# Optimization experiments

Hardware: AMD Instinct MI355X
Metric: run time of the kernel (lower is better)

The kernel has to match this reference:

```python
import jax, jax.numpy as jnp
import numpy as np

N = 50000; E = 120000; FN = 64; EA = 16; R = 4; H = 4; HID = 128; L = 3
NIDS = 10001; IDE = 32; RED = 8; NG = 64; NC = 10; KH = 128; GRID = 5; ORD = 3
EDIM = EA + RED; FFH = 256; GK = GRID + ORD


def layernorm(x, w, b):
    m = x.mean(-1, keepdims=True)
    v = ((x - m) ** 2).mean(-1, keepdims=True)
    return (x - m) / jnp.sqrt(v + 1e-5) * w + b


def b_splines(x, grid, k):
    # x: (B, in); grid: (in, G + 2k + 1) -> bases: (B, in, G + k)
    xe = x[..., None]
    bases = ((xe >= grid[:, :-1]) & (xe < grid[:, 1:])).astype(x.dtype)
    for j in range(1, k + 1):
        bases = ((xe - grid[:, :-(j + 1)]) / (grid[:, j:-1] - grid[:, :-(j + 1)]) * bases[..., :-1]
                 + (grid[:, j + 1:] - xe) / (grid[:, j + 1:] - grid[:, 1:-j]) * bases[..., 1:])
    return bases


def kan_linear(x, bw, sw, sc, grid):
    base = jax.nn.silu(x) @ bw.T
    B = b_splines(x, grid, ORD)
    return base + jnp.einsum('big,oig->bo', B, sw * sc[..., None])


def make_grid(in_features):
    h = 2.0 / GRID
    g = np.arange(-ORD, GRID + ORD + 1) * h - 1.0
    return jnp.asarray(np.tile(g, (in_features, 1)), dtype=jnp.float32)


def setup_inputs():
    key = jax.random.key(0)
    ks = jax.random.split(key, 24)
    s = 0.02
    inp = {}
    inp['x'] = jax.random.normal(ks[0], (N, FN), jnp.float32)
    inp['edge_attr'] = jax.random.normal(ks[1], (E, EA), jnp.float32)
    inp['id_token'] = jax.random.randint(ks[2], (N,), 0, NIDS)
    inp['edge_index'] = jax.random.randint(ks[3], (2, E), 0, N)
    inp['edge_type'] = jax.random.randint(ks[4], (E,), 0, R)
    inp['batch'] = jnp.sort(jax.random.randint(ks[5], (N,), 0, NG))
    inp['id_emb_table'] = jax.random.normal(ks[6], (NIDS, IDE)) * s
    inp['in_proj_w'] = jax.random.normal(ks[7], (HID, FN + IDE)) * s
    inp['in_proj_b'] = jnp.zeros((HID,))
    inp['rel_emb'] = jax.random.normal(ks[8], (L, R, RED)) * s
    inp['lin_l_w'] = jax.random.normal(ks[9], (L, R, H * HID, HID)) * s
    inp['lin_l_b'] = jnp.zeros((L, R, H * HID))
    inp['lin_r_w'] = jax.random.normal(ks[10], (L, R, H * HID, HID)) * s
    inp['lin_r_b'] = jnp.zeros((L, R, H * HID))
    inp['lin_edge_w'] = jax.random.normal(ks[11], (L, R, H * HID, EDIM)) * s
    inp['att_w'] = jax.random.normal(ks[12], (L, R, H, HID)) * s
    inp['conv_bias'] = jnp.zeros((L, R, HID))
    inp['rel_gate'] = jnp.zeros((L, R))
    inp['norm1_w'] = jnp.ones((L, HID)); inp['norm1_b'] = jnp.zeros((L, HID))
    inp['norm2_w'] = jnp.ones((L, HID)); inp['norm2_b'] = jnp.zeros((L, HID))
    inp['ffn_w1'] = jax.random.normal(ks[13], (L, FFH, HID)) * s
    inp['ffn_b1'] = jnp.zeros((L, FFH))
    inp['ffn_w2'] = jax.random.normal(ks[14], (L, HID, FFH)) * s
    inp['ffn_b2'] = jnp.zeros((L, HID))
    inp['readout_norm_w'] = jnp.ones((2 * HID,)); inp['readout_norm_b'] = jnp.zeros((2 * HID,))
    inp['base_w1'] = jax.random.normal(ks[15], (KH, 2 * HID)) * s
    inp['spline_w1'] = jax.random.normal(ks[16], (KH, 2 * HID, GK)) * s
    inp['spline_scaler1'] = jnp.ones((KH, 2 * HID))
    inp['grid1'] = make_grid(2 * HID)
    inp['base_w2'] = jax.random.normal(ks[17], (NC, KH)) * s
    inp['spline_w2'] = jax.random.normal(ks[18], (NC, KH, GK)) * s
    inp['spline_scaler2'] = jnp.ones((NC, KH))
    inp['grid2'] = make_grid(KH)
    return inp


def reference(x, edge_attr, id_token, edge_index, edge_type, batch,
              id_emb_table, in_proj_w, in_proj_b, rel_emb,
              lin_l_w, lin_l_b, lin_r_w, lin_r_b, lin_edge_w, att_w, conv_bias,
              rel_gate, norm1_w, norm1_b, norm2_w, norm2_b,
              ffn_w1, ffn_b1, ffn_w2, ffn_b2, readout_norm_w, readout_norm_b,
              base_w1, spline_w1, spline_scaler1, grid1,
              base_w2, spline_w2, spline_scaler2, grid2):
    src, dst = edge_index[0], edge_index[1]
    h = jnp.concatenate([x, id_emb_table[id_token]], -1)
    h = jax.nn.silu(h @ in_proj_w.T + in_proj_b)  # input_proj (eval: no dropout)
    for l in range(L):
        gate = jax.nn.softmax(rel_gate[l])  # all relations present w.h.p.
        h_msg = jnp.zeros_like(h)
        for r in range(R):
            maskf = (edge_type == r).astype(h.dtype)
            ea = jnp.concatenate([edge_attr, jnp.broadcast_to(rel_emb[l, r], (E, RED))], -1)
            xl = (h @ lin_l_w[l, r].T + lin_l_b[l, r]).reshape(N, H, HID)
            xr = (h @ lin_r_w[l, r].T + lin_r_b[l, r]).reshape(N, H, HID)
            ee = (ea @ lin_edge_w[l, r].T).reshape(E, H, HID)
            sfeat = jax.nn.leaky_relu(xl[src] + xr[dst] + ee, negative_slope=0.2)
            logit = jnp.einsum('ehc,hc->eh', sfeat, att_w[l, r])
            logit = jnp.where(maskf[:, None] > 0, logit, -1e9)
            m = jax.ops.segment_max(logit, dst, num_segments=N)
            a = jnp.exp(logit - m[dst]) * maskf[:, None]
            den = jax.ops.segment_sum(a, dst, num_segments=N)
            a = a / jnp.where(den == 0, 1.0, den)[dst]
            out = jax.ops.segment_sum(a[:, :, None] * xl[src], dst, num_segments=N)
            out = out.mean(1) + conv_bias[l, r]  # concat=False -> head mean
            h_msg = h_msg + gate[r] * out
        h = layernorm(h + h_msg, norm1_w[l], norm1_b[l])
        f = jax.nn.silu(h @ ffn_w1[l].T + ffn_b1[l]) @ ffn_w2[l].T + ffn_b2[l]
        h = layernorm(h + f, norm2_w[l], norm2_b[l])
    cnt = jax.ops.segment_sum(jnp.ones((N,), h.dtype), batch, num_segments=NG)
    hmean = jax.ops.segment_sum(h, batch, num_segments=NG) / jnp.maximum(cnt, 1.0)[:, None]
    hmax = jax.ops.segment_max(h, batch, num_segments=NG)
    g = layernorm(jnp.concatenate([hmean, hmax], -1), readout_norm_w, readout_norm_b)
    z = kan_linear(g, base_w1, spline_w1, spline_scaler1, grid1)
    logits = kan_linear(z, base_w2, spline_w2, spline_scaler2, grid2)
    return logits
```

## Files before the change

### kernel.cpp

```cpp
#include <hip/hip_runtime.h>
#include <math.h>

#define NN 50000
#define NE 120000
#define FN 64
#define NEA 16
#define NR 4
#define NH 4
#define HID 128
#define NL 3
#define IDE 32
#define RED 8
#define NG 64
#define NC 10
#define KH 128
#define FFH 256
#define NBIN (NR * NN)
#define SCAN_BLK ((NBIN + 1023) / 1024)
#define CAPS 32768
#define CAPH 9216

typedef short bf16x8 __attribute__((ext_vector_type(8)));
typedef float f32x4 __attribute__((ext_vector_type(4)));

__device__ __forceinline__ unsigned short f2b(float f) {
  unsigned u = __float_as_uint(f);
  unsigned r = (u + 0x7FFFu + ((u >> 16) & 1u)) >> 16;
  return (unsigned short)r;
}
__device__ __forceinline__ float b2f(unsigned short b) {
  return __uint_as_float((unsigned)b << 16);
}

__global__ void cvt_bf16(const float* __restrict__ s, unsigned short* __restrict__ d, int n4) {
  int i = blockIdx.x * blockDim.x + threadIdx.x;
  if (i >= n4) return;
  float4 v = ((const float4*)s)[i];
  ushort4 o;
  o.x = f2b(v.x); o.y = f2b(v.y); o.z = f2b(v.z); o.w = f2b(v.w);
  ((ushort4*)d)[i] = o;
}

template <int KT>
__device__ __forceinline__ void gemm_direct(
    const unsigned short* __restrict__ A, const int* __restrict__ rowlist,
    const unsigned short* __restrict__ W, const float* __restrict__ bias,
    float* __restrict__ Cf, unsigned short* __restrict__ Cb,
    int nrows, int mout, int act, int rowBase, int colBase) {
  constexpr int NK = KT / 32;
  __shared__ unsigned short Es[64][136];
  int t = threadIdx.x;
  int lane = t & 63, w = t >> 6;
  int wm = w >> 1, wn = w & 1;
  int q = lane >> 4, mr = lane & 15;

  const unsigned short* ap[2];
#pragma unroll
  for (int mt = 0; mt < 2; ++mt) {
    int gr = rowBase + wm * 32 + mt * 16 + mr;
    int cg = (gr < nrows) ? gr : 0;
    int ar = rowlist ? rowlist[cg] : cg;
    ap[mt] = A + (size_t)ar * KT + q * 8;
  }
  const unsigned short* wp[4];
#pragma unroll
  for (int nt = 0; nt < 4; ++nt)
    wp[nt] = W + (size_t)(colBase + wn * 64 + nt * 16 + mr) * KT + q * 8;

  f32x4 acc[2][4] = {};
#pragma unroll
  for (int k = 0; k < NK; ++k) {
    bf16x8 af[2], bfr[4];
#pragma unroll
    for (int mt = 0; mt < 2; ++mt) af[mt] = *(const bf16x8*)(ap[mt] + k * 32);
#pragma unroll
    for (int nt = 0; nt < 4; ++nt) bfr[nt] = *(const bf16x8*)(wp[nt] + k * 32);
#pragma unroll
    for (int mt = 0; mt < 2; ++mt)
#pragma unroll
      for (int nt = 0; nt < 4; ++nt)
        acc[mt][nt] = __builtin_amdgcn_mfma_f32_16x16x32_bf16(af[mt], bfr[nt], acc[mt][nt], 0, 0, 0);
  }

  float bv[4];
#pragma unroll
  for (int nt = 0; nt < 4; ++nt) bv[nt] = bias[colBase + wn * 64 + nt * 16 + mr];

  if (Cf) {
#pragma unroll
    for (int mt = 0; mt < 2; ++mt)
#pragma unroll
      for (int nt = 0; nt < 4; ++nt)
#pragma unroll
        for (int r = 0; r < 4; ++r) {
          int row = rowBase + wm * 32 + mt * 16 + q * 4 + r;
          int col = colBase + wn * 64 + nt * 16 + mr;
          if (row < nrows) {
            float v = acc[mt][nt][r] + bv[nt];
            if (act) v = v / (1.f + expf(-v));
            Cf[(size_t)row * mout + col] = v;
            if (Cb) Cb[(size_t)row * mout + col] = f2b(v);
          }
        }
  } else {
#pragma unroll
    for (int mt = 0; mt < 2; ++mt)
#pragma unroll
      for (int nt = 0; nt < 4; ++nt)
#pragma unroll
        for (int r = 0; r < 4; ++r) {
          float v = acc[mt][nt][r] + bv[nt];
          if (act) v = v / (1.f + expf(-v));
          Es[wm * 32 + mt * 16 + q * 4 + r][wn * 64 + nt * 16 + mr] = f2b(v);
        }
    __syncthreads();
    int rl = t >> 2, co = (t & 3) * 32;
    int grow = rowBase + rl;
    if (grow < nrows) {
      unsigned short* dst = Cb + (size_t)grow * mout + colBase + co;
#pragma unroll
      for (int j = 0; j < 4; ++j)
        *(bf16x8*)(dst + j * 8) = *(const bf16x8*)&Es[rl][co + j * 8];
    }
  }
}

template <int KT>
__global__ __launch_bounds__(256, 2) void gemm_bf16_t(
    const unsigned short* __restrict__ A, const unsigned short* __restrict__ W,
    const float* __restrict__ bias, float* __restrict__ Cf, unsigned short* __restrict__ Cb,
    int nrows, int mout, int act, int ncol) {
  int nbr = (nrows + 63) >> 6;
  int rpx = (nbr + 7) >> 3;
  int xcd = blockIdx.x & 7, j = blockIdx.x >> 3;
  int rowT = xcd * rpx + j / ncol;
  int cy = j - (j / ncol) * ncol;
  if (rowT >= nbr) return;
  gemm_direct<KT>(A, nullptr, W, bias, Cf, Cb, nrows, mout, act, rowT * 64, cy * 128);
}

__global__ __launch_bounds__(256, 2) void conv_solo_all(
    const unsigned short* __restrict__ hbf,
    const int* __restrict__ srclist, const int* __restrict__ hotlist,
    const int* __restrict__ cnts,
    const unsigned short* __restrict__ Wl, const float* __restrict__ bl,
    const unsigned short* __restrict__ Wr, const float* __restrict__ br,
    unsigned short* __restrict__ xlb, unsigned short* __restrict__ xrh,
    const int* __restrict__ solosrc, const int* __restrict__ solodst,
    const unsigned short* __restrict__ wsum, const float* __restrict__ bsum,
    const float* __restrict__ gate, float* __restrict__ hmsg) {
  int t = threadIdx.x, lane = t & 63, w = t >> 6;
  int wm = w >> 1, wn = w & 1, q = lane >> 4, mr = lane & 15;
  for (int tid = blockIdx.x;; tid += gridDim.x) {
    int rem = tid, seg = 0, nrows = 0;
    for (; seg < 12; ++seg) {
      int n, tseg;
      if (seg < 8) {
        int r = seg >> 1;
        n = (seg & 1) ? cnts[64 + r * 16] : cnts[128 + r * 16];
        int cap = (seg & 1) ? CAPH : CAPS;
        if (n > cap) n = cap;
        tseg = ((n + 63) >> 6) * 4;
      } else {
        n = cnts[(seg - 8) * 16];
        tseg = (n + 63) >> 6;
      }
      if (rem < tseg) { nrows = n; break; }
      rem -= tseg;
    }
    if (seg == 12) return;
    if (seg < 8) {
      int r = seg >> 1, sel = seg & 1;
      int rt = rem >> 2, ct = rem & 3;
      const int* list = (sel ? hotlist : srclist) + r * NN;
      const unsigned short* W = (sel ? Wr : Wl) + (size_t)r * 512 * 128;
      const float* bias = (sel ? br : bl) + (size_t)r * 512;
      unsigned short* C = sel ? (xrh + (size_t)r * CAPH * 512) : (xlb + (size_t)r * CAPS * 512);
      gemm_direct<128>(hbf, list, W, bias, nullptr, C, nrows, 512, 0, rt * 64, ct * 128);
    } else {
      int r = seg - 8;
      int rowBase = rem * 64;
      const unsigned short* ap[2];
#pragma unroll
      for (int mt = 0; mt < 2; ++mt) {
        int gr = rowBase + wm * 32 + mt * 16 + mr;
        int idx = (gr < nrows) ? solosrc[r * NN + gr] : 0;
        ap[mt] = hbf + (size_t)idx * HID + q * 8;
      }
      const unsigned short* wp[4];
#pragma unroll
      for (int nt = 0; nt < 4; ++nt)
        wp[nt] = wsum + (size_t)r * 16384 + (size_t)(wn * 64 + nt * 16 + mr) * HID + q * 8;
      f32x4 acc[2][4] = {};
#pragma unroll
      for (int k = 0; k < 4; ++k) {
        bf16x8 af[2], bfr[4];
#pragma unroll
        for (int mt = 0; mt < 2; ++mt) af[mt] = *(const bf16x8*)(ap[mt] + k * 32);
#pragma unroll
        for (int nt = 0; nt < 4; ++nt) bfr[nt] = *(const bf16x8*)(wp[nt] + k * 32);
#pragma unroll
        for (int mt = 0; mt < 2; ++mt)
#pragma unroll
          for (int nt = 0; nt < 4; ++nt)
            acc[mt][nt] = __builtin_amdgcn_mfma_f32_16x16x32_bf16(af[mt], bfr[nt], acc[mt][nt], 0, 0, 0);
      }
      float g4 = gate[r] * 0.25f;
      float bv[4];
#pragma unroll
      for (int nt = 0; nt < 4; ++nt) bv[nt] = bsum[r * 128 + wn * 64 + nt * 16 + mr];
#pragma unroll
      for (int mt = 0; mt < 2; ++mt)
#pragma unroll
        for (int rr = 0; rr < 4; ++rr) {
          int row = rowBase + wm * 32 + mt * 16 + q * 4 + rr;
          if (row < nrows) {
            int dst = solodst[r * NN + row];
#pragma unroll
            for (int nt = 0; nt < 4; ++nt) {
              int col = wn * 64 + nt * 16 + mr;
              atomicAdd(&hmsg[(size_t)dst * HID + col], g4 * (acc[mt][nt][rr] + bv[nt]));
            }
          }
        }
    }
    __syncthreads();
  }
}

__global__ void wsum_build(const float* __restrict__ linlw, const float* __restrict__ linlb,
                           unsigned short* __restrict__ wsum, float* __restrict__ bsum) {
  int i = blockIdx.x * blockDim.x + threadIdx.x;
  if (i >= NL * NR * 128 * 128) return;
  int k = i & 127, o = (i >> 7) & 127, lr = i >> 14;
  float s = 0.f;
#pragma unroll
  for (int h = 0; h < NH; ++h) s += linlw[((size_t)lr * 512 + h * 128 + o) * 128 + k];
  wsum[i] = f2b(s);
  if (k == 0) {
    float b = 0.f;
#pragma unroll
    for (int h = 0; h < NH; ++h) b += linlb[(size_t)lr * 512 + h * 128 + o];
    bsum[lr * 128 + o] = b;
  }
}

__global__ __launch_bounds__(256, 2) void layer_tail(
    float* __restrict__ h, float* __restrict__ hmsg, const float* __restrict__ cb,
    const float* __restrict__ n1w, const float* __restrict__ n1b,
    const unsigned short* __restrict__ W1, const float* __restrict__ b1,
    const unsigned short* __restrict__ W2, const float* __restrict__ b2,
    const float* __restrict__ n2w, const float* __restrict__ n2b,
    unsigned short* __restrict__ hbfout) {
  __shared__ __align__(16) char smem[64 * 136 * 2 + 64 * 264 * 2];
  unsigned short (*Y)[136] = (unsigned short (*)[136])smem;
  unsigned short (*F1)[264] = (unsigned short (*)[264])(smem + 64 * 136 * 2);
  float (*Ef)[132] = (float (*)[132])(smem + 64 * 136 * 2);
  int nbr = (NN + 63) >> 6;
  int rpx = (nbr + 7) >> 3;
  int xcd = blockIdx.x & 7, j = blockIdx.x >> 3;
  int rowT = xcd * rpx + j;
  if (rowT >= nbr) return;
  int rowBase = rowT * 64;

  int t = threadIdx.x;
  int lane = t & 63, w = t >> 6;
  int wm = w >> 1, wn = w & 1;
  int q = lane >> 4, mr = lane & 15;

  float y0r[16], y1r[16];
  {
    float w0 = n1w[lane], w1 = n1w[64 + lane];
    float bb0 = n1b[lane], bb1 = n1b[64 + lane];
    float c0 = cb[lane], c1 = cb[64 + lane];
#pragma unroll
    for (int it = 0; it < 16; ++it) {
      int rr = it * 4 + w;
      int grow = rowBase + rr;
      if (grow < NN) {
        size_t base = (size_t)grow * HID;
        float x0 = h[base + lane] + hmsg[base + lane] + c0;
        float x1 = h[base + 64 + lane] + hmsg[base + 64 + lane] + c1;
        hmsg[base + lane] = 0.f;
        hmsg[base + 64 + lane] = 0.f;
        float s = x0 + x1;
#pragma unroll
        for (int o = 32; o > 0; o >>= 1) s += __shfl_xor(s, o, 64);
        float mean = s * (1.f / 128.f);
        float d0 = x0 - mean, d1 = x1 - mean;
        float v = d0 * d0 + d1 * d1;
#pragma unroll
        for (int o = 32; o > 0; o >>= 1) v += __shfl_xor(v, o, 64);
        float inv = 1.f / sqrtf(v * (1.f / 128.f) + 1e-5f);
        float y0 = d0 * inv * w0 + bb0;
        float y1 = d1 * inv * w1 + bb1;
        y0r[it] = y0;
        y1r[it] = y1;
        Y[rr][lane] = f2b(y0);
        Y[rr][64 + lane] = f2b(y1);
      } else {
        y0r[it] = 0.f;
        y1r[it] = 0.f;
        Y[rr][lane] = 0;
        Y[rr][64 + lane] = 0;
      }
    }
  }
  __syncthreads();

  bf16x8 a[2][4];
#pragma unroll
  for (int mt = 0; mt < 2; ++mt)
#pragma unroll
    for (int k = 0; k < 4; ++k)
      a[mt][k] = *(const bf16x8*)&Y[wm * 32 + mt * 16 + mr][k * 32 + q * 8];

#pragma unroll
  for (int ph = 0; ph < 2; ++ph) {
    const unsigned short* wp[4];
#pragma unroll
    for (int nt = 0; nt < 4; ++nt)
      wp[nt] = W1 + (size_t)(ph * 128 + wn * 64 + nt * 16 + mr) * HID + q * 8;
    f32x4 acc[2][4] = {};
#pragma unroll
    for (int k = 0; k < 4; ++k) {
      bf16x8 bfr[4];
#pragma unroll
      for (int nt = 0; nt < 4; ++nt) bfr[nt] = *(const bf16x8*)(wp[nt] + k * 32);
#pragma unroll
      for (int mt = 0; mt < 2; ++mt)
#pragma unroll
        for (int nt = 0; nt < 4; ++nt)
          acc[mt][nt] = __builtin_amdgcn_mfma_f32_16x16x32_bf16(a[mt][k], bfr[nt], acc[mt][nt], 0, 0, 0);
    }
    float bv[4];
#pragma unroll
    for (int nt = 0; nt < 4; ++nt) bv[nt] = b1[ph * 128 + wn * 64 + nt * 16 + mr];
#pragma unroll
    for (int mt = 0; mt < 2; ++mt)
#pragma unroll
      for (int nt = 0; nt < 4; ++nt)
#pragma unroll
        for (int r = 0; r < 4; ++r) {
          float v = acc[mt][nt][r] + bv[nt];
          v = v / (1.f + expf(-v));
          F1[wm * 32 + mt * 16 + q * 4 + r][ph * 128 + wn * 64 + nt * 16 + mr] = f2b(v);
        }
  }
  __syncthreads();

  const unsigned short* wp2[4];
#pragma unroll
  for (int nt = 0; nt < 4; ++nt)
    wp2[nt] = W2 + (size_t)(wn * 64 + nt * 16 + mr) * FFH + q * 8;
  f32x4 acc2[2][4] = {};
#pragma unroll
  for (int k = 0; k < 8; ++k) {
    bf16x8 af[2], bfr[4];
#pragma unroll
    for (int mt = 0; mt < 2; ++mt)
      af[mt] = *(const bf16x8*)&F1[wm * 32 + mt * 16 + mr][k * 32 + q * 8];
#pragma unroll
    for (int nt = 0; nt < 4; ++nt) bfr[nt] = *(const bf16x8*)(wp2[nt] + k * 32);
#pragma unroll
    for (int mt = 0; mt < 2; ++mt)
#pragma unroll
      for (int nt = 0; nt < 4; ++nt)
        acc2[mt][nt] = __builtin_amdgcn_mfma_f32_16x16x32_bf16(af[mt], bfr[nt], acc2[mt][nt], 0, 0, 0);
  }
  __syncthreads();

  float bv2[4];
#pragma unroll
  for (int nt = 0; nt < 4; ++nt) bv2[nt] = b2[wn * 64 + nt * 16 + mr];
#pragma unroll
  for (int mt = 0; mt < 2; ++mt)
#pragma unroll
    for (int nt = 0; nt < 4; ++nt)
#pragma unroll
      for (int r = 0; r < 4; ++r)
        Ef[wm * 32 + mt * 16 + q * 4 + r][wn * 64 + nt * 16 + mr] = acc2[mt][nt][r] + bv2[nt];
  __syncthreads();

  float w0 = n2w[lane], w1 = n2w[64 + lane];
  float bb0 = n2b[lane], bb1 = n2b[64 + lane];
#pragma unroll
  for (int it = 0; it < 16; ++it) {
    int rr = it * 4 + w;
    int grow = rowBase + rr;
    if (grow >= NN) continue;
    size_t base = (size_t)grow * HID;
    float x0 = y0r[it] + Ef[rr][lane];
    float x1 = y1r[it] + Ef[rr][64 + lane];
    float s = x0 + x1;
#pragma unroll
    for (int o = 32; o > 0; o >>= 1) s += __shfl_xor(s, o, 64);
    float mean = s * (1.f / 128.f);
    float d0 = x0 - mean, d1 = x1 - mean;
    float v = d0 * d0 + d1 * d1;
#pragma unroll
    for (int o = 32; o > 0; o >>= 1) v += __shfl_xor(v, o, 64);
    float inv = 1.f / sqrtf(v * (1.f / 128.f) + 1e-5f);
    float y0 = d0 * inv * w0 + bb0;
    float y1 = d1 * inv * w1 + bb1;
    h[base + lane] = y0;
    h[base + 64 + lane] = y1;
    hbfout[base + lane] = f2b(y0);
    hbfout[base + 64 + lane] = f2b(y1);
  }
}

__global__ void build_xin_bf(const float* __restrict__ x, const int* __restrict__ idtok,
                             const float* __restrict__ emb, unsigned short* __restrict__ xin) {
  int i = blockIdx.x * blockDim.x + threadIdx.x;
  if (i >= NN * 96) return;
  int n = i / 96, k = i - n * 96;
  float v = (k < FN) ? x[(size_t)n * FN + k] : emb[(size_t)idtok[n] * IDE + (k - FN)];
  xin[i] = f2b(v);
}

__global__ void hist_bin(const int* __restrict__ ei, const int* __restrict__ et,
                         int* __restrict__ bcnt) {
  int e = blockIdx.x * blockDim.x + threadIdx.x;
  if (e >= NE) return;
  atomicAdd(&bcnt[et[e] * NN + ei[NE + e]], 1);
}
__global__ __launch_bounds__(256) void scan1(const int* __restrict__ cnt,
                                             int* __restrict__ pos, int* __restrict__ bsum) {
  __shared__ int lds[256];
  int b = blockIdx.x, t = threadIdx.x;
  int base = b * 1024 + t * 4;
  int v[4];
#pragma unroll
  for (int j = 0; j < 4; ++j) v[j] = (base + j < NBIN) ? cnt[base + j] : 0;
  int tot = v[0] + v[1] + v[2] + v[3];
  lds[t] = tot;
  __syncthreads();
  for (int off = 1; off < 256; off <<= 1) {
    int x = (t >= off) ? lds[t - off] : 0;
    __syncthreads();
    lds[t] += x;
    __syncthreads();
  }
  if (t == 255) bsum[b] = lds[255];
  int run = lds[t] - tot;
#pragma unroll
  for (int j = 0; j < 4; ++j) {
    if (base + j < NBIN) pos[base + j] = run;
    run += v[j];
  }
}
__global__ __launch_bounds__(256) void scan2(int* __restrict__ bsum) {
  __shared__ int lds[256];
  int t = threadIdx.x;
  int v = (t < SCAN_BLK) ? bsum[t] : 0;
  lds[t] = v;
  __syncthreads();
  for (int off = 1; off < 256; off <<= 1) {
    int x = (t >= off) ? lds[t - off] : 0;
    __syncthreads();
    lds[t] += x;
    __syncthreads();
  }
  if (t < SCAN_BLK) bsum[t] = lds[t] - v;
}
__global__ void scan3(int* __restrict__ pos, const int* __restrict__ bsum,
                      const int* __restrict__ cnt) {
  int i = blockIdx.x * blockDim.x + threadIdx.x;
  if (i >= NBIN) return;
  pos[i] += bsum[i >> 10];
  if (i == NBIN - 1) pos[NBIN] = pos[i] + cnt[i];
}
__global__ void scatter_bin(const int* __restrict__ ei, const int* __restrict__ et,
                            const int* __restrict__ csroff, int* __restrict__ cur,
                            int* __restrict__ elist) {
  int e = blockIdx.x * blockDim.x + threadIdx.x;
  if (e >= NE) return;
  int bin = et[e] * NN + ei[NE + e];
  int p = atomicAdd(&cur[bin], 1);
  elist[csroff[bin] + p] = e;
}
__global__ void sort_bins(const int* __restrict__ csroff, int* __restrict__ elist) {
  int b = blockIdx.x * blockDim.x + threadIdx.x;
  if (b >= NBIN) return;
  int s = csroff[b], e = csroff[b + 1];
  for (int i = s + 1; i < e; ++i) {
    int key = elist[i];
    int j = i - 1;
    while (j >= s && elist[j] > key) { elist[j + 1] = elist[j]; --j; }
    elist[j + 1] = key;
  }
}
__global__ void gather_edge(const int* __restrict__ ei, const int* __restrict__ elist,
                            const float* __restrict__ eattr,
                            int* __restrict__ rsrc, float* __restrict__ eacsr) {
  int p = blockIdx.x * blockDim.x + threadIdx.x;
  if (p >= NE) return;
  int e = elist[p];
  rsrc[p] = ei[e];
  const float4* s = (const float4*)(eattr + (size_t)e * NEA);
  float4* d = (float4*)(eacsr + (size_t)p * NEA);
#pragma unroll
  for (int j = 0; j < 4; ++j) d[j] = s[j];
}
__global__ void mark_hotsrc(const int* __restrict__ csroff, const int* __restrict__ rsrc,
                            int* __restrict__ srcflag) {
  int b = blockIdx.x * blockDim.x + threadIdx.x;
  if (b >= NBIN) return;
  int s = csroff[b], e = csroff[b + 1];
  if (e - s < 2) return;
  int rel = b / NN;
  for (int p = s; p < e; ++p) srcflag[rel * NN + rsrc[p]] = 1;
}
__global__ void build_src_o(const int* __restrict__ srcflag, const int* __restrict__ srcpos,
                            int* __restrict__ srclist, int* __restrict__ srcmap) {
  int b = blockIdx.x * blockDim.x + threadIdx.x;
  if (b >= NBIN) return;
  if (srcflag[b]) {
    int rel = b / NN;
    int pos = srcpos[b] - srcpos[rel * NN];
    srcmap[b] = pos;
    srclist[rel * NN + pos] = b - rel * NN;
  }
}
__global__ void fincnt(const int* __restrict__ srcpos, int* __restrict__ nsrc) {
  int r = threadIdx.x;
  if (r < NR) nsrc[r * 16] = srcpos[(r + 1) * NN] - srcpos[r * NN];
}
__global__ void remap_rsrc(const int* __restrict__ csroff, const int* __restrict__ rsrc,
                           const int* __restrict__ srcmap, int* __restrict__ rsrcx) {
  int p = blockIdx.x * blockDim.x + threadIdx.x;
  if (p >= NE) return;
  int rel = (p >= csroff[NN]) + (p >= csroff[2 * NN]) + (p >= csroff[3 * NN]);
  rsrcx[p] = srcmap[rel * NN + rsrc[p]];
}
__global__ __launch_bounds__(256) void build_hot(
    const int* __restrict__ csroff, const int* __restrict__ rsrc,
    int* __restrict__ nsolo, int* __restrict__ nhot,
    int* __restrict__ solosrc, int* __restrict__ solodst, int* __restrict__ hotlist) {
  __shared__ int wsc[4][4], whc[4][4];
  __shared__ int sbase[4], hbase[4];
  int t = threadIdx.x, wave = t >> 6, lane = t & 63;
  int b = blockIdx.x * 256 + t;
  bool valid = b < NBIN;
  int cnt = 0, rel = 0, s = 0;
  if (valid) { s = csroff[b]; cnt = csroff[b + 1] - s; rel = b / NN; }
  bool solo = valid && cnt == 1;
  bool hot = valid && cnt >= 2;
#pragma unroll
  for (int rr = 0; rr < 4; ++rr) {
    unsigned long long ms = __ballot(solo && rel == rr);
    unsigned long long mh = __ballot(hot && rel == rr);
    if (lane == 0) { wsc[wave][rr] = __popcll(ms); whc[wave][rr] = __popcll(mh); }
  }
  __syncthreads();
  if (t < 4) {
    int ssum = wsc[0][t] + wsc[1][t] + wsc[2][t] + wsc[3][t];
    int hsum = whc[0][t] + whc[1][t] + whc[2][t] + whc[3][t];
    sbase[t] = ssum ? atomicAdd(&nsolo[t * 16], ssum) : 0;
    hbase[t] = hsum ? atomicAdd(&nhot[t * 16], hsum) : 0;
  }
  __syncthreads();
#pragma unroll
  for (int rr = 0; rr < 4; ++rr) {
    unsigned long long ms = __ballot(solo && rel == rr);
    if (solo && rel == rr) {
      int before = 0;
#pragma unroll
      for (int wv = 0; wv < 4; ++wv) if (wv < wave) before += wsc[wv][rr];
      int pos = sbase[rr] + before + __popcll(ms & ((1ull << lane) - 1ull));
      solosrc[rr * NN + pos] = rsrc[s];
      solodst[rr * NN + pos] = b - rr * NN;
    }
    unsigned long long mh = __ballot(hot && rel == rr);
    if (hot && rel == rr) {
      int before = 0;
#pragma unroll
      for (int wv = 0; wv < 4; ++wv) if (wv < wave) before += whc[wv][rr];
      int pos = hbase[rr] + before + __popcll(mh & ((1ull << lane) - 1ull));
      hotlist[rr * NN + pos] = b - rr * NN;
    }
  }
}

__global__ void gate_cb_all(const float* __restrict__ rg, const float* __restrict__ cbias,
                            float* __restrict__ gate, float* __restrict__ cb) {
  __shared__ float g[NR];
  int l = blockIdx.x, t = threadIdx.x;
  const float* rgl = rg + l * NR;
  if (t == 0) {
    float mx = rgl[0];
    for (int r = 1; r < NR; ++r) mx = fmaxf(mx, rgl[r]);
    float s = 0.f, tmp[NR];
    for (int r = 0; r < NR; ++r) { tmp[r] = expf(rgl[r] - mx); s += tmp[r]; }
    for (int r = 0; r < NR; ++r) { g[r] = tmp[r] / s; gate[l * NR + r] = g[r]; }
  }
  __syncthreads();
  float c = 0.f;
  for (int r = 0; r < NR; ++r) c += g[r] * cbias[(size_t)l * NR * HID + r * HID + t];
  cb[l * HID + t] = c;
}

__global__ __launch_bounds__(256) void edge_all(
    const int* __restrict__ csroff, const int* __restrict__ rsrcx,
    const float* __restrict__ eacsr, const float* __restrict__ relembp,
    const float* __restrict__ wedgep, const float* __restrict__ attwp,
    const unsigned short* __restrict__ xlb, const unsigned short* __restrict__ xrh,
    const int* __restrict__ hotlist, const int* __restrict__ nhot,
    float* __restrict__ hmsg, const float* __restrict__ gate, int rel) {
  __shared__ float lds[4][128];
  int wave = threadIdx.x >> 6, lane = threadIdx.x & 63;
  float g4 = gate[rel] * 0.25f;
  int hh = wave;
  float wreg[2][24], areg[2];
#pragma unroll
  for (int j = 0; j < 2; ++j) {
    int col = hh * 128 + j * 64 + lane;
    const float* wp = wedgep + (size_t)col * 24;
#pragma unroll
    for (int k = 0; k < 24; ++k) wreg[j][k] = wp[k];
    areg[j] = attwp[col];
  }
  float evr0 = 0.f, evr1 = 0.f;
#pragma unroll
  for (int k = 0; k < 8; ++k) {
    float rk = relembp[k];
    evr0 += rk * wreg[0][NEA + k];
    evr1 += rk * wreg[1][NEA + k];
  }
  int nh = nhot[rel * 16];
  for (int wi = blockIdx.x; wi < nh; wi += gridDim.x) {
    int dst = hotlist[rel * NN + wi];
    int s = csroff[rel * NN + dst], e = csroff[rel * NN + dst + 1];
    {
      const unsigned short* xrp = xrh + (size_t)wi * 512;
      float xr0 = b2f(xrp[hh * 128 + lane]);
      float xr1 = b2f(xrp[hh * 128 + 64 + lane]);
      float m = -3.4e38f, den = 0.f, acc0 = 0.f, acc1 = 0.f;
      for (int p = s; p < e; ++p) {
        int src = rsrcx[p];
        const float* eap = eacsr + (size_t)p * NEA;
        float eev0 = evr0, eev1 = evr1;
#pragma unroll
        for (int k = 0; k < NEA; ++k) {
          float er = eap[k];
          eev0 += er * wreg[0][k];
          eev1 += er * wreg[1][k];
        }
        float xl0 = b2f(xlb[(size_t)src * 512 + hh * 128 + lane]);
        float xl1 = b2f(xlb[(size_t)src * 512 + hh * 128 + 64 + lane]);
        float s0 = xl0 + xr0 + eev0; s0 = (s0 > 0.f) ? s0 : 0.2f * s0;
        float s1 = xl1 + xr1 + eev1; s1 = (s1 > 0.f) ? s1 : 0.2f * s1;
        float lg = s0 * areg[0] + s1 * areg[1];
#pragma unroll
        for (int o = 32; o > 0; o >>= 1) lg += __shfl_xor(lg, o, 64);
        float mn = fmaxf(m, lg);
        float sc = expf(m - mn);
        float ex = expf(lg - mn);
        den = den * sc + ex;
        acc0 = acc0 * sc + ex * xl0;
        acc1 = acc1 * sc + ex * xl1;
        m = mn;
      }
      float wgt = g4 / den;
      lds[wave][lane] = acc0 * wgt;
      lds[wave][64 + lane] = acc1 * wgt;
    }
    __syncthreads();
    if (wave < 2) {
      int d = wave * 64 + lane;
      float v = lds[0][d] + lds[1][d] + lds[2][d] + lds[3][d];
      hmsg[(size_t)dst * HID + d] += v;
    }
    __syncthreads();
  }
}

__global__ void group_bounds(const int* __restrict__ batch, int* __restrict__ gstart) {
  int g = threadIdx.x + blockIdx.x * blockDim.x;
  if (g > NG) return;
  int lo = 0, hi = NN;
  while (lo < hi) {
    int mid = (lo + hi) >> 1;
    if (batch[mid] < g) lo = mid + 1; else hi = mid;
  }
  gstart[g] = lo;
}
__global__ __launch_bounds__(128) void readout_part2(
    const float* __restrict__ h, const int* __restrict__ gstart,
    float* __restrict__ psum, float* __restrict__ pmax) {
  int g = blockIdx.x, s = blockIdx.y, t = threadIdx.x;
  int r0 = gstart[g], r1 = gstart[g + 1];
  float acc = 0.f, mx = -3.4e38f;
  for (int row = r0 + s; row < r1; row += 8) {
    float v = h[(size_t)row * HID + t];
    acc += v;
    mx = fmaxf(mx, v);
  }
  psum[((size_t)g * 8 + s) * HID + t] = acc;
  pmax[((size_t)g * 8 + s) * HID + t] = mx;
}
__global__ __launch_bounds__(256) void readout_final(
    const int* __restrict__ gstart, const float* __restrict__ psum,
    const float* __restrict__ pmax, const float* __restrict__ w,
    const float* __restrict__ b, float* __restrict__ g) {
  int bg = blockIdx.x, t = threadIdx.x;
  __shared__ float red[256];
  float c = fmaxf((float)(gstart[bg + 1] - gstart[bg]), 1.f);
  float x;
  if (t < HID) {
    float ssum = 0.f;
    for (int s = 0; s < 8; ++s) ssum += psum[((size_t)bg * 8 + s) * HID + t];
    x = ssum / c;
  } else {
    float mx = -3.4e38f;
    for (int s = 0; s < 8; ++s) mx = fmaxf(mx, pmax[((size_t)bg * 8 + s) * HID + (t - HID)]);
    x = mx;
  }
  red[t] = x;
  __syncthreads();
  for (int s = 128; s > 0; s >>= 1) {
    if (t < s) red[t] += red[t + s];
    __syncthreads();
  }
  float mean = red[0] * (1.f / 256.f);
  __syncthreads();
  float d = x - mean;
  red[t] = d * d;
  __syncthreads();
  for (int s = 128; s > 0; s >>= 1) {
    if (t < s) red[t] += red[t + s];
    __syncthreads();
  }
  float inv = 1.f / sqrtf(red[0] * (1.f / 256.f) + 1e-5f);
  g[(size_t)bg * 256 + t] = d * inv * w[t] + b[t];
}

__device__ __forceinline__ void bspline8(float x, const float* __restrict__ t,
                                         float* __restrict__ out) {
  float bs[11];
#pragma unroll
  for (int j = 0; j < 11; ++j) bs[j] = (x >= t[j] && x < t[j + 1]) ? 1.f : 0.f;
#pragma unroll
  for (int k = 1; k <= 3; ++k) {
    for (int j = 0; j < 11 - k; ++j) {
      bs[j] = (x - t[j]) / (t[j + k] - t[j]) * bs[j] +
              (t[j + k + 1] - x) / (t[j + k + 1] - t[j + 1]) * bs[j + 1];
    }
  }
#pragma unroll
  for (int j = 0; j < 8; ++j) out[j] = bs[j];
}

__global__ __launch_bounds__(128) void kan1_part(
    const float* __restrict__ g, const float* __restrict__ bw,
    const float* __restrict__ sw, const float* __restrict__ sc,
    const float* __restrict__ grid, float* __restrict__ zpart) {
  int bg = blockIdx.x, ch = blockIdx.y, t = threadIdx.x;
  int base = ch * 32;
  __shared__ float B[32][8];
  __shared__ float sg[32];
  if (t < 32) {
    float x = g[(size_t)bg * 256 + base + t];
    sg[t] = x / (1.f + expf(-x));
    bspline8(x, grid + (size_t)(base + t) * 12, B[t]);
  }
  __syncthreads();
  float acc = 0.f;
  for (int i = 0; i < 32; ++i) {
    int col = base + i;
    acc += sg[i] * bw[(size_t)t * 256 + col];
    const float* swp = sw + ((size_t)t * 256 + col) * 8;
    float sp = 0.f;
#pragma unroll
    for (int k = 0; k < 8; ++k) sp += B[i][k] * swp[k];
    acc += sp * sc[(size_t)t * 256 + col];
  }
  zpart[((size_t)ch * NG + bg) * KH + t] = acc;
}

__global__ __launch_bounds__(128) void kan2(
    const float* __restrict__ zpart, const float* __restrict__ bw,
    const float* __restrict__ sw, const float* __restrict__ sc,
    const float* __restrict__ grid, float* __restrict__ out) {
  int bg = blockIdx.x, t = threadIdx.x;
  __shared__ float B[128][8];
  __shared__ float sz[128];
  float x = 0.f;
  for (int ch = 0; ch < 8; ++ch) x += zpart[((size_t)ch * NG + bg) * KH + t];
  sz[t] = x / (1.f + expf(-x));
  bspline8(x, grid + (size_t)t * 12, B[t]);
  __syncthreads();
  if (t < NC) {
    float acc = 0.f;
    for (int i = 0; i < 128; ++i) {
      acc += sz[i] * bw[(size_t)t * 128 + i];
      const float* swp = sw + ((size_t)t * 128 + i) * 8;
      float sp = 0.f;
#pragma unroll
      for (int k = 0; k < 8; ++k) sp += B[i][k] * swp[k];
      acc += sp * sc[(size_t)t * 128 + i];
    }
    out[(size_t)bg * NC + t] = acc;
  }
}

extern "C" void kernel_launch(void* const* d_in, const int* in_sizes, int n_in,
                              void* d_out, int out_size, void* d_ws, size_t ws_size,
                              hipStream_t stream) {
  const float* x       = (const float*)d_in[0];
  const float* eattr   = (const float*)d_in[1];
  const int*   idtok   = (const int*)d_in[2];
  const int*   ei      = (const int*)d_in[3];
  const int*   etype   = (const int*)d_in[4];
  const int*   batch   = (const int*)d_in[5];
  const float* idemb   = (const float*)d_in[6];
  const float* inw     = (const float*)d_in[7];
  const float* inb     = (const float*)d_in[8];
  const float* relemb  = (const float*)d_in[9];
  const float* linlw   = (const float*)d_in[10];
  const float* linlb   = (const float*)d_in[11];
  const float* linrw   = (const float*)d_in[12];
  const float* linrb   = (const float*)d_in[13];
  const float* linew   = (const float*)d_in[14];
  const float* attw    = (const float*)d_in[15];
  const float* convb   = (const float*)d_in[16];
  const float* relgate = (const float*)d_in[17];
  const float* n1w     = (const float*)d_in[18];
  const float* n1b     = (const float*)d_in[19];
  const float* n2w     = (const float*)d_in[20];
  const float* n2b     = (const float*)d_in[21];
  const float* f1w     = (const float*)d_in[22];
  const float* f1bias  = (const float*)d_in[23];
  const float* f2w     = (const float*)d_in[24];
  const float* f2bias  = (const float*)d_in[25];
  const float* rnw     = (const float*)d_in[26];
  const float* rnb     = (const float*)d_in[27];
  const float* bw1     = (const float*)d_in[28];
  const float* sw1     = (const float*)d_in[29];
  const float* sc1     = (const float*)d_in[30];
  const float* grid1   = (const float*)d_in[31];
  const float* bw2     = (const float*)d_in[32];
  const float* sw2     = (const float*)d_in[33];
  const float* sc2     = (const float*)d_in[34];
  const float* grid2   = (const float*)d_in[35];
  float* out = (float*)d_out;
  (void)in_sizes; (void)n_in; (void)out_size; (void)ws_size;

  char* p = (char*)d_ws;
  auto alloc = [&](size_t bytes) { void* q = (void*)p; p += (bytes + 255) & ~(size_t)255; return q; };
  float* h    = (float*)alloc((size_t)NN * HID * 4);
  float* hmsg = (float*)alloc((size_t)NN * HID * 4);
  unsigned short* hbf = (unsigned short*)alloc((size_t)NN * HID * 2);
  unsigned short* xlb = (unsigned short*)alloc((size_t)NR * CAPS * 512 * 2);
  unsigned short* xrh = (unsigned short*)alloc((size_t)NR * CAPH * 512 * 2);
  int* elist = (int*)alloc((size_t)NE * 4);
  int* rsrc  = (int*)alloc((size_t)NE * 4);
  int* rsrcx = (int*)alloc((size_t)NE * 4);
  float* eacsr = (float*)alloc((size_t)NE * NEA * 4);
  int* bcnt  = (int*)alloc((size_t)NBIN * 8 + 8);
  int* cur   = bcnt + NBIN;
  int* csroff = (int*)alloc((size_t)(NBIN + 1) * 4);
  int* srcpos = (int*)alloc((size_t)(NBIN + 1) * 4);
  int* bsum  = (int*)alloc((size_t)SCAN_BLK * 4);
  int* hotlist = (int*)alloc((size_t)NR * NN * 4);
  int* solosrc = (int*)alloc((size_t)NR * NN * 4);
  int* solodst = (int*)alloc((size_t)NR * NN * 4);
  int* srclist = (int*)alloc((size_t)NR * NN * 4);
  int* srcflag = (int*)alloc((size_t)NBIN * 4);
  int* srcmap  = (int*)alloc((size_t)NBIN * 4);
  int* cnts    = (int*)alloc(1024);
  int* nsolo   = cnts;
  int* nhot    = cnts + 64;
  int* nsrc    = cnts + 128;
  unsigned short* linlwb = (unsigned short*)alloc((size_t)NL * NR * 512 * 128 * 2);
  unsigned short* linrwb = (unsigned short*)alloc((size_t)NL * NR * 512 * 128 * 2);
  unsigned short* f1wb   = (unsigned short*)alloc((size_t)NL * 256 * 128 * 2);
  unsigned short* f2wb   = (unsigned short*)alloc((size_t)NL * 128 * 256 * 2);
  unsigned short* inwb   = (unsigned short*)alloc((size_t)128 * 96 * 2);
  unsigned short* wsumb  = (unsigned short*)alloc((size_t)NL * NR * 128 * 128 * 2);
  float* bsumf = (float*)alloc((size_t)NL * NR * 128 * 4);
  float* gate = (float*)alloc(NL * NR * 4);
  float* cb   = (float*)alloc(NL * HID * 4);
  int* gstart = (int*)alloc((size_t)(NG + 1) * 4);
  float* psum = (float*)alloc((size_t)NG * 8 * HID * 4);
  float* pmax = (float*)alloc((size_t)NG * 8 * HID * 4);
  float* zpart = (float*)alloc((size_t)8 * NG * KH * 4);
  float* g = (float*)alloc((size_t)NG * 256 * 4);
  unsigned short* xinbf = xlb;

  const int NB64 = (NN + 63) / 64;
  const int RPX = (NB64 + 7) / 8;

  {
    int n;
    n = NL * NR * 512 * 128 / 4;
    cvt_bf16<<<(n + 255) / 256, 256, 0, stream>>>(linlw, linlwb, n);
    cvt_bf16<<<(n + 255) / 256, 256, 0, stream>>>(linrw, linrwb, n);
    n = NL * 256 * 128 / 4;
    cvt_bf16<<<(n + 255) / 256, 256, 0, stream>>>(f1w, f1wb, n);
    cvt_bf16<<<(n + 255) / 256, 256, 0, stream>>>(f2w, f2wb, n);
    n = 128 * 96 / 4;
    cvt_bf16<<<(n + 255) / 256, 256, 0, stream>>>(inw, inwb, n);
  }
  wsum_build<<<(NL * NR * 128 * 128 + 255) / 256, 256, 0, stream>>>(linlw, linlb, wsumb, bsumf);

  hipMemsetAsync(bcnt, 0, (size_t)NBIN * 8 + 8, stream);
  hipMemsetAsync(srcflag, 0, (size_t)NBIN * 4, stream);
  hipMemsetAsync(cnts, 0, 1024, stream);
  hist_bin<<<(NE + 255) / 256, 256, 0, stream>>>(ei, etype, bcnt);
  scan1<<<SCAN_BLK, 256, 0, stream>>>(bcnt, csroff, bsum);
  scan2<<<1, 256, 0, stream>>>(bsum);
  scan3<<<(NBIN + 255) / 256, 256, 0, stream>>>(csroff, bsum, bcnt);
  scatter_bin<<<(NE + 255) / 256, 256, 0, stream>>>(ei, etype, csroff, cur, elist);
  sort_bins<<<(NBIN + 255) / 256, 256, 0, stream>>>(csroff, elist);
  gather_edge<<<(NE + 255) / 256, 256, 0, stream>>>(ei, elist, eattr, rsrc, eacsr);
  mark_hotsrc<<<(NBIN + 255) / 256, 256, 0, stream>>>(csroff, rsrc, srcflag);
  scan1<<<SCAN_BLK, 256, 0, stream>>>(srcflag, srcpos, bsum);
  scan2<<<1, 256, 0, stream>>>(bsum);
  scan3<<<(NBIN + 255) / 256, 256, 0, stream>>>(srcpos, bsum, srcflag);
  build_src_o<<<(NBIN + 255) / 256, 256, 0, stream>>>(srcflag, srcpos, srclist, srcmap);
  fincnt<<<1, 64, 0, stream>>>(srcpos, nsrc);
  remap_rsrc<<<(NE + 255) / 256, 256, 0, stream>>>(csroff, rsrc, srcmap, rsrcx);
  build_hot<<<(NBIN + 255) / 256, 256, 0, stream>>>(csroff, rsrc, nsolo, nhot,
                                                    solosrc, solodst, hotlist);
  gate_cb_all<<<NL, 128, 0, stream>>>(relgate, convb, gate, cb);

  build_xin_bf<<<(NN * 96 + 255) / 256, 256, 0, stream>>>(x, idtok, idemb, xinbf);
  gemm_bf16_t<96><<<8 * RPX, 256, 0, stream>>>(xinbf, inwb, inb, h, hbf, NN, 128, 1, 1);

  hipMemsetAsync(hmsg, 0, (size_t)NN * HID * 4, stream);
  for (int l = 0; l < NL; ++l) {
    conv_solo_all<<<4096, 256, 0, stream>>>(
        hbf, srclist, hotlist, cnts,
        linlwb + (size_t)l * NR * 512 * 128, linlb + (size_t)l * NR * 512,
        linrwb + (size_t)l * NR * 512 * 128, linrb + (size_t)l * NR * 512,
        xlb, xrh,
        solosrc, solodst,
        wsumb + (size_t)l * NR * 16384, bsumf + (size_t)l * NR * 128,
        gate + l * NR, hmsg);
    for (int r = 0; r < NR; ++r) {
      int lr = l * NR + r;
      edge_all<<<4096, 256, 0, stream>>>(
          csroff, rsrcx, eacsr, relemb + (size_t)lr * RED,
          linew + (size_t)lr * 512 * 24,
          attw + (size_t)lr * 512,
          xlb + (size_t)r * CAPS * 512, xrh + (size_t)r * CAPH * 512,
          hotlist, nhot, hmsg, gate + l * NR, r);
    }
    layer_tail<<<8 * RPX, 256, 0, stream>>>(
        h, hmsg, cb + l * HID, n1w + l * HID, n1b + l * HID,
        f1wb + (size_t)l * 256 * 128, f1bias + (size_t)l * 256,
        f2wb + (size_t)l * 128 * 256, f2bias + (size_t)l * 128,
        n2w + l * HID, n2b + l * HID, hbf);
  }

  group_bounds<<<1, 128, 0, stream>>>(batch, gstart);
  readout_part2<<<dim3(NG, 8), 128, 0, stream>>>(h, gstart, psum, pmax);
  readout_final<<<NG, 256, 0, stream>>>(gstart, psum, pmax, rnw, rnb, g);
  kan1_part<<<dim3(NG, 8), 128, 0, stream>>>(g, bw1, sw1, sc1, grid1, zpart);
  kan2<<<NG, 128, 0, stream>>>(zpart, bw2, sw2, sc2, grid2, out);
}
```

Baseline: 1.060 ms.

## Merge per-relation edge kernels into one launch and fold hot-source marking into gather

The four per-relation edge attention launches per layer become a single kernel in which the block index selects the relation. Because several relations can now update the same destination row at once, the plain read-modify-write on hmsg becomes an atomicAdd. The mark_hotsrc pass is folded into gather_edge, which sets the source flag per edge using the bin size, and conv_solo_all gets twice as many blocks. The aim is fewer launches and better occupancy, at the cost of float atomics and nondeterministic summation order.

```diff
diff --git a/kernel.cpp b/kernel.cpp
--- a/kernel.cpp
+++ b/kernel.cpp
@@ -491,26 +491,22 @@
     elist[j + 1] = key;
   }
 }
-__global__ void gather_edge(const int* __restrict__ ei, const int* __restrict__ elist,
+__global__ void gather_edge(const int* __restrict__ ei, const int* __restrict__ et,
+                            const int* __restrict__ elist, const int* __restrict__ csroff,
                             const float* __restrict__ eattr,
-                            int* __restrict__ rsrc, float* __restrict__ eacsr) {
+                            int* __restrict__ rsrc, float* __restrict__ eacsr,
+                            int* __restrict__ srcflag) {
   int p = blockIdx.x * blockDim.x + threadIdx.x;
   if (p >= NE) return;
   int e = elist[p];
-  rsrc[p] = ei[e];
+  int src = ei[e];
+  rsrc[p] = src;
   const float4* s = (const float4*)(eattr + (size_t)e * NEA);
   float4* d = (float4*)(eacsr + (size_t)p * NEA);
 #pragma unroll
   for (int j = 0; j < 4; ++j) d[j] = s[j];
-}
-__global__ void mark_hotsrc(const int* __restrict__ csroff, const int* __restrict__ rsrc,
-                            int* __restrict__ srcflag) {
-  int b = blockIdx.x * blockDim.x + threadIdx.x;
-  if (b >= NBIN) return;
-  int s = csroff[b], e = csroff[b + 1];
-  if (e - s < 2) return;
-  int rel = b / NN;
-  for (int p = s; p < e; ++p) srcflag[rel * NN + rsrc[p]] = 1;
+  int bin = et[e] * NN + ei[NE + e];
+  if (csroff[bin + 1] - csroff[bin] >= 2) srcflag[et[e] * NN + src] = 1;
 }
 __global__ void build_src_o(const int* __restrict__ srcflag, const int* __restrict__ srcpos,
                             int* __restrict__ srclist, int* __restrict__ srcmap) {
@@ -601,17 +597,25 @@
   cb[l * HID + t] = c;
 }
 
-__global__ __launch_bounds__(256) void edge_all(
+__global__ __launch_bounds__(256) void edge_merged(
     const int* __restrict__ csroff, const int* __restrict__ rsrcx,
-    const float* __restrict__ eacsr, const float* __restrict__ relembp,
-    const float* __restrict__ wedgep, const float* __restrict__ attwp,
+    const float* __restrict__ eacsr, const float* __restrict__ relembL,
+    const float* __restrict__ wedgeL, const float* __restrict__ attwL,
     const unsigned short* __restrict__ xlb, const unsigned short* __restrict__ xrh,
     const int* __restrict__ hotlist, const int* __restrict__ nhot,
-    float* __restrict__ hmsg, const float* __restrict__ gate, int rel) {
+    float* __restrict__ hmsg, const float* __restrict__ gate) {
   __shared__ float lds[4][128];
   int wave = threadIdx.x >> 6, lane = threadIdx.x & 63;
+  int rel = blockIdx.x & 3;
+  int b0 = blockIdx.x >> 2;
+  int bstride = gridDim.x >> 2;
   float g4 = gate[rel] * 0.25f;
   int hh = wave;
+  const float* wedgep = wedgeL + (size_t)rel * 512 * 24;
+  const float* attwp = attwL + (size_t)rel * 512;
+  const float* relembp = relembL + rel * RED;
+  const unsigned short* xlbase = xlb + (size_t)rel * CAPS * 512;
+  const unsigned short* xrbase = xrh + (size_t)rel * CAPH * 512;
   float wreg[2][24], areg[2];
 #pragma unroll
   for (int j = 0; j < 2; ++j) {
@@ -629,11 +633,11 @@
     evr1 += rk * wreg[1][NEA + k];
   }
   int nh = nhot[rel * 16];
-  for (int wi = blockIdx.x; wi < nh; wi += gridDim.x) {
+  for (int wi = b0; wi < nh; wi += bstride) {
     int dst = hotlist[rel * NN + wi];
     int s = csroff[rel * NN + dst], e = csroff[rel * NN + dst + 1];
     {
-      const unsigned short* xrp = xrh + (size_t)wi * 512;
+      const unsigned short* xrp = xrbase + (size_t)wi * 512;
       float xr0 = b2f(xrp[hh * 128 + lane]);
       float xr1 = b2f(xrp[hh * 128 + 64 + lane]);
       float m = -3.4e38f, den = 0.f, acc0 = 0.f, acc1 = 0.f;
@@ -647,8 +651,8 @@
           eev0 += er * wreg[0][k];
           eev1 += er * wreg[1][k];
         }
-        float xl0 = b2f(xlb[(size_t)src * 512 + hh * 128 + lane]);
-        float xl1 = b2f(xlb[(size_t)src * 512 + hh * 128 + 64 + lane]);
+        float xl0 = b2f(xlbase[(size_t)src * 512 + hh * 128 + lane]);
+        float xl1 = b2f(xlbase[(size_t)src * 512 + hh * 128 + 64 + lane]);
         float s0 = xl0 + xr0 + eev0; s0 = (s0 > 0.f) ? s0 : 0.2f * s0;
         float s1 = xl1 + xr1 + eev1; s1 = (s1 > 0.f) ? s1 : 0.2f * s1;
         float lg = s0 * areg[0] + s1 * areg[1];
@@ -670,7 +674,7 @@
     if (wave < 2) {
       int d = wave * 64 + lane;
       float v = lds[0][d] + lds[1][d] + lds[2][d] + lds[3][d];
-      hmsg[(size_t)dst * HID + d] += v;
+      atomicAdd(&hmsg[(size_t)dst * HID + d], v);
     }
     __syncthreads();
   }
@@ -914,8 +918,8 @@
   scan3<<<(NBIN + 255) / 256, 256, 0, stream>>>(csroff, bsum, bcnt);
   scatter_bin<<<(NE + 255) / 256, 256, 0, stream>>>(ei, etype, csroff, cur, elist);
   sort_bins<<<(NBIN + 255) / 256, 256, 0, stream>>>(csroff, elist);
-  gather_edge<<<(NE + 255) / 256, 256, 0, stream>>>(ei, elist, eattr, rsrc, eacsr);
-  mark_hotsrc<<<(NBIN + 255) / 256, 256, 0, stream>>>(csroff, rsrc, srcflag);
+  gather_edge<<<(NE + 255) / 256, 256, 0, stream>>>(ei, etype, elist, csroff, eattr,
+                                                    rsrc, eacsr, srcflag);
   scan1<<<SCAN_BLK, 256, 0, stream>>>(srcflag, srcpos, bsum);
   scan2<<<1, 256, 0, stream>>>(bsum);
   scan3<<<(NBIN + 255) / 256, 256, 0, stream>>>(srcpos, bsum, srcflag);
@@ -931,7 +935,7 @@
 
   hipMemsetAsync(hmsg, 0, (size_t)NN * HID * 4, stream);
   for (int l = 0; l < NL; ++l) {
-    conv_solo_all<<<4096, 256, 0, stream>>>(
+    conv_solo_all<<<8192, 256, 0, stream>>>(
         hbf, srclist, hotlist, cnts,
         linlwb + (size_t)l * NR * 512 * 128, linlb + (size_t)l * NR * 512,
         linrwb + (size_t)l * NR * 512 * 128, linrb + (size_t)l * NR * 512,
@@ -939,15 +943,12 @@
         solosrc, solodst,
         wsumb + (size_t)l * NR * 16384, bsumf + (size_t)l * NR * 128,
         gate + l * NR, hmsg);
-    for (int r = 0; r < NR; ++r) {
-      int lr = l * NR + r;
-      edge_all<<<4096, 256, 0, stream>>>(
-          csroff, rsrcx, eacsr, relemb + (size_t)lr * RED,
-          linew + (size_t)lr * 512 * 24,
-          attw + (size_t)lr * 512,
-          xlb + (size_t)r * CAPS * 512, xrh + (size_t)r * CAPH * 512,
-          hotlist, nhot, hmsg, gate + l * NR, r);
-    }
+    edge_merged<<<4096, 256, 0, stream>>>(
+        csroff, rsrcx, eacsr,
+        relemb + (size_t)l * NR * RED,
+        linew + (size_t)l * NR * 512 * 24,
+        attw + (size_t)l * NR * 512,
+        xlb, xrh, hotlist, nhot, hmsg, gate + l * NR);
     layer_tail<<<8 * RPX, 256, 0, stream>>>(
         h, hmsg, cb + l * HID, n1w + l * HID, n1b + l * HID,
         f1wb + (size_t)l * 256 * 128, f1bias + (size_t)l * 256,
```

After: 1.018 ms. -3.9%, faster.
